# Kernel tuning notes

Hardware: AMD Instinct MI355X
Metric: run time of the kernel (lower is better)

Reference implementation:

```python
import jax, jax.numpy as jnp
import numpy as np


def setup_inputs() -> dict:
    key = jax.random.key(0)
    ks = jax.random.split(key, 7)
    B, N, F, H = 128, 64, 128, 128
    s1 = 1.0 / np.sqrt(2 * N)  # torch Linear default-ish scaling
    s2 = 1.0 / np.sqrt(H)
    return {
        "agent_features": jax.random.normal(ks[0], (B, N, F), dtype=jnp.float32),
        "W1": jax.random.normal(ks[1], (2 * N, H), dtype=jnp.float32) * s1,
        "b1": jax.random.normal(ks[2], (H,), dtype=jnp.float32) * s1,
        "W2": jax.random.normal(ks[3], (H, H), dtype=jnp.float32) * s2,
        "b2": jax.random.normal(ks[4], (H,), dtype=jnp.float32) * s2,
        "w3": jax.random.normal(ks[5], (H,), dtype=jnp.float32) * s2,
        "b3": jax.random.normal(ks[6], (1,), dtype=jnp.float32) * s2,
        "mixing_weights": jnp.ones((N,), dtype=jnp.float32) / N,
    }


def reference(agent_features, W1, b1, W2, b2, w3, b3, mixing_weights):
    N = mixing_weights.shape[0]
    f = agent_features[:, :, :N]  # [B, N, N] (first num_agents features)
    # Split first Linear's weight into the i-half and j-half of the concat:
    # concat([f_i, f_j]) @ W1 == f_i @ W1[:N] + f_j @ W1[N:]
    Ai = jnp.einsum('bnf,fh->bnh', f, W1[:N])   # contribution of agent i
    Aj = jnp.einsum('bnf,fh->bnh', f, W1[N:])   # contribution of agent j
    h1 = jax.nn.relu(Ai[:, :, None, :] + Aj[:, None, :, :] + b1)  # [B,N,N,H]
    h2 = jax.nn.relu(jnp.einsum('bijh,hk->bijk', h1, W2) + b2)    # [B,N,N,H]
    correlations = jax.nn.sigmoid(jnp.einsum('bijh,h->bij', h2, w3) + b3[0])
    weights = jax.nn.softmax(mixing_weights, axis=0)
    return correlations, weights
```

## Files before the change

### kernel.cpp

```cpp
#include <hip/hip_runtime.h>
#include <hip/hip_bf16.h>


typedef __bf16 bf16x8 __attribute__((ext_vector_type(8)));
typedef float f32x4 __attribute__((ext_vector_type(4)));

#define B_SZ 128
#define N_SZ 64
#define H_SZ 128

__global__ __launch_bounds__(256) void setup_kernel(
    const float* __restrict__ af, const float* __restrict__ W1,
    const float* __restrict__ b1, const float* __restrict__ W2,
    const float* __restrict__ mw, float* __restrict__ AiP,
    float* __restrict__ Aj, unsigned short* __restrict__ W2T,
    float* __restrict__ outw)
{
  const int blk = blockIdx.x;
  const int tid = threadIdx.x;

  if (blk < 2048) {
    __shared__ float fl[4 * 64];
    const int bn0 = blk << 2;
    fl[tid] = af[((bn0 + (tid >> 6)) << 7) + (tid & 63)];
    __syncthreads();
    const int h    = tid & 127;
    const int half = tid >> 7;
    const float* Wp = W1 + ((half << 6) << 7) + h;
    float acc0 = 0.f, acc1 = 0.f, acc2 = 0.f, acc3 = 0.f;
#pragma unroll
    for (int fq = 0; fq < 16; ++fq) {
      const float w0 = Wp[(fq * 4 + 0) << 7];
      const float w1v = Wp[(fq * 4 + 1) << 7];
      const float w2v = Wp[(fq * 4 + 2) << 7];
      const float w3v = Wp[(fq * 4 + 3) << 7];
      const float4 f0 = *(const float4*)&fl[0 * 64 + (fq << 2)];
      const float4 f1 = *(const float4*)&fl[1 * 64 + (fq << 2)];
      const float4 f2 = *(const float4*)&fl[2 * 64 + (fq << 2)];
      const float4 f3 = *(const float4*)&fl[3 * 64 + (fq << 2)];
      acc0 = fmaf(f0.x, w0, fmaf(f0.y, w1v, fmaf(f0.z, w2v, fmaf(f0.w, w3v, acc0))));
      acc1 = fmaf(f1.x, w0, fmaf(f1.y, w1v, fmaf(f1.z, w2v, fmaf(f1.w, w3v, acc1))));
      acc2 = fmaf(f2.x, w0, fmaf(f2.y, w1v, fmaf(f2.z, w2v, fmaf(f2.w, w3v, acc2))));
      acc3 = fmaf(f3.x, w0, fmaf(f3.y, w1v, fmaf(f3.z, w2v, fmaf(f3.w, w3v, acc3))));
    }
    if (half == 0) {
      const float bb = b1[h];
      AiP[((bn0 + 0) << 7) + h] = acc0 + bb;
      AiP[((bn0 + 1) << 7) + h] = acc1 + bb;
      AiP[((bn0 + 2) << 7) + h] = acc2 + bb;
      AiP[((bn0 + 3) << 7) + h] = acc3 + bb;
    } else {
      Aj[((bn0 + 0) << 7) + h] = acc0;
      Aj[((bn0 + 1) << 7) + h] = acc1;
      Aj[((bn0 + 2) << 7) + h] = acc2;
      Aj[((bn0 + 3) << 7) + h] = acc3;
    }
  } else if (blk < 2112) {
    int idx = ((blk - 2048) << 8) + tid;
    int k = idx >> 7, n = idx & 127;
    unsigned u = __float_as_uint(W2[idx]);
    u += 0x7fffu + ((u >> 16) & 1u);
    W2T[(n << 7) + k] = (unsigned short)(u >> 16);
  } else {
    if (tid < 64) {
      float v = mw[tid];
      float m = v;
      for (int off = 32; off > 0; off >>= 1) m = fmaxf(m, __shfl_xor(m, off));
      float e = expf(v - m);
      float s = e;
      for (int off = 32; off > 0; off >>= 1) s += __shfl_xor(s, off);
      outw[tid] = e / s;
    }
  }
}

__global__ __launch_bounds__(512, 2) void corr_kernel(
    const float* __restrict__ AiP, const float* __restrict__ Aj,
    const unsigned short* __restrict__ W2T,
    const float* __restrict__ b2, const float* __restrict__ w3,
    const float* __restrict__ b3, float* __restrict__ out)
{
  __shared__ __align__(16) unsigned short W2s[128 * 128];
  __shared__ __align__(16) float AjF[64 * 132];
  __shared__ __align__(16) float AiF[32 * 132];
  __shared__ float b2s[128], w3s[128];
  __shared__ float part[2][2][128];

  const int tid  = threadIdx.x;
  const int lane = tid & 63;
  const int wave = tid >> 6;
  const int c = lane & 15, g = lane >> 4;
  const int wm = wave & 1;
  const int wn = wave >> 1;

  const int blk = blockIdx.x;
  const int b   = blk >> 1;
  const int ih  = blk & 1;
  const int ip0 = ih << 4;

  {
    const uint4* src = (const uint4*)W2T;
#pragma unroll
    for (int it = 0; it < 4; ++it) {
      const int idx = (it << 9) + tid;
      const int n = idx >> 4, e = idx & 15;
      const uint4 v = src[idx];
      *(uint4*)&W2s[(n << 7) + ((e ^ (n & 15)) << 3)] = v;
    }
  }
  {
    const float4* src = (const float4*)(Aj + (b << 13));
#pragma unroll
    for (int p = 0; p < 4; ++p) {
      const int idx = (p << 9) + tid;
      const int r = idx >> 5, u = idx & 31;
      *(float4*)&AjF[r * 132 + (u << 2)] = src[idx];
    }
    const float4* srcA = (const float4*)(AiP + (((b << 6) + (ih << 5)) << 7));
#pragma unroll
    for (int p = 0; p < 2; ++p) {
      const int idx = (p << 9) + tid;
      const int r = idx >> 5, u = idx & 31;
      *(float4*)&AiF[r * 132 + (u << 2)] = srcA[idx];
    }
    if (tid < 128) b2s[tid] = b2[tid];
    else if (tid < 256) w3s[tid - 128] = w3[tid - 128];
  }

  const float bias3 = b3[0];
  const int i_sel = wn >> 1;

  __syncthreads();

  bf16x8 w2r[4][4];
#pragma unroll
  for (int mt = 0; mt < 4; ++mt)
#pragma unroll
    for (int kt = 0; kt < 4; ++kt) {
      const int es = ((kt << 2) + g) ^ c;
      w2r[mt][kt] = *(const bf16x8*)&W2s[(((wm << 6) + (mt << 4) + c) << 7) + (es << 3)];
    }
  f32x4 ajr[4][2][2];
#pragma unroll
  for (int kt = 0; kt < 4; ++kt)
#pragma unroll
    for (int tn = 0; tn < 2; ++tn) {
      const int j = ((wn << 5) + (tn << 4) + c) & 63;
      const float* ajb = &AjF[j * 132 + (g << 3) + (kt << 5)];
      ajr[kt][tn][0] = *(const f32x4*)(ajb);
      ajr[kt][tn][1] = *(const f32x4*)(ajb + 4);
    }

  for (int t = 0; t < 16; ++t) {
    const float* aib = &AiF[((t << 1) + i_sel) * 132 + (g << 3)];

    f32x4 acc[4][2];
#pragma unroll
    for (int mt = 0; mt < 4; ++mt) {
      const f32x4 bv = *(const f32x4*)&b2s[(wm << 6) + (mt << 4) + (g << 2)];
      acc[mt][0] = bv;
      acc[mt][1] = bv;
    }

#pragma unroll
    for (int kt = 0; kt < 4; ++kt) {
      const f32x4 a0 = *(const f32x4*)(aib + (kt << 5));
      const f32x4 a1 = *(const f32x4*)(aib + (kt << 5) + 4);
      bf16x8 hv[2];
#pragma unroll
      for (int tn = 0; tn < 2; ++tn) {
        const f32x4 h0 = a0 + ajr[kt][tn][0];
        const f32x4 h1v = a1 + ajr[kt][tn][1];
#pragma unroll
        for (int e = 0; e < 4; ++e) {
          hv[tn][e]     = (__bf16)fmaxf(h0[e], 0.f);
          hv[tn][e + 4] = (__bf16)fmaxf(h1v[e], 0.f);
        }
      }
#pragma unroll
      for (int mt = 0; mt < 4; ++mt)
#pragma unroll
        for (int tn = 0; tn < 2; ++tn)
          acc[mt][tn] = __builtin_amdgcn_mfma_f32_16x16x32_bf16(
              w2r[mt][kt], hv[tn], acc[mt][tn], 0, 0, 0);
    }

    float s0 = 0.f, s1 = 0.f;
#pragma unroll
    for (int mt = 0; mt < 4; ++mt) {
      const f32x4 wv3 = *(const f32x4*)&w3s[(wm << 6) + (mt << 4) + (g << 2)];
#pragma unroll
      for (int p = 0; p < 4; ++p) {
        s0 = fmaf(fmaxf(acc[mt][0][p], 0.f), wv3[p], s0);
        s1 = fmaf(fmaxf(acc[mt][1][p], 0.f), wv3[p], s1);
      }
    }
    s0 += __shfl_xor(s0, 16);
    s0 += __shfl_xor(s0, 32);
    s1 += __shfl_xor(s1, 16);
    s1 += __shfl_xor(s1, 32);

    const int pb = t & 1;
    if (g == 0) {
      part[pb][wm][(wn << 5) + c]      = s0;
      part[pb][wm][(wn << 5) + 16 + c] = s1;
    }

    __syncthreads();

    if (tid < 128) {
      const float v = part[pb][0][tid] + part[pb][1][tid] + bias3;
      out[(b << 12) + ((ip0 + t) << 7) + tid] = 1.f / (1.f + __expf(-v));
    }
  }
}

extern "C" void kernel_launch(void* const* d_in, const int* in_sizes, int n_in,
                              void* d_out, int out_size, void* d_ws,
                              size_t ws_size, hipStream_t stream)
{
  const float* af = (const float*)d_in[0];
  const float* W1 = (const float*)d_in[1];
  const float* b1 = (const float*)d_in[2];
  const float* W2 = (const float*)d_in[3];
  const float* b2 = (const float*)d_in[4];
  const float* w3 = (const float*)d_in[5];
  const float* b3 = (const float*)d_in[6];
  const float* mw = (const float*)d_in[7];
  float* out = (float*)d_out;

  float* AiP = (float*)d_ws;
  float* Aj  = AiP + B_SZ * N_SZ * H_SZ;
  unsigned short* W2T = (unsigned short*)(Aj + B_SZ * N_SZ * H_SZ);

  setup_kernel<<<2113, 256, 0, stream>>>(af, W1, b1, W2, mw, AiP, Aj, W2T,
                                         out + B_SZ * N_SZ * N_SZ);
  corr_kernel<<<256, 512, 0, stream>>>(AiP, Aj, W2T, b2, w3, b3, out);
}
```

Measured before the change: 102.9 us.

## Fuse first-layer projection and W2 conversion into the correlation kernel

Merges the setup kernel into the main kernel. Each block now computes its own Aj (all 64 rows) and Ai (its 32 rows) projections from agent features in shared memory, and loads W2 straight from global memory, converting it to bf16 into registers. This removes a kernel launch and the workspace round trip for AiP, Aj and W2T. In exchange, each batch's Aj projection is computed twice (once per i-half block), and every block does strided fp32 reads of W2 and W1 through a 64-entry register array, which may raise register pressure.

After: 105.7 us. 1.03x slower.

```diff
diff --git a/kernel.cpp b/kernel.cpp
--- a/kernel.cpp
+++ b/kernel.cpp
@@ -5,82 +5,14 @@
 typedef __bf16 bf16x8 __attribute__((ext_vector_type(8)));
 typedef float f32x4 __attribute__((ext_vector_type(4)));
 
-#define B_SZ 128
-#define N_SZ 64
-#define H_SZ 128
-
-__global__ __launch_bounds__(256) void setup_kernel(
+__global__ __launch_bounds__(512, 2) void fused_kernel(
     const float* __restrict__ af, const float* __restrict__ W1,
     const float* __restrict__ b1, const float* __restrict__ W2,
-    const float* __restrict__ mw, float* __restrict__ AiP,
-    float* __restrict__ Aj, unsigned short* __restrict__ W2T,
-    float* __restrict__ outw)
+    const float* __restrict__ b2, const float* __restrict__ w3,
+    const float* __restrict__ b3, const float* __restrict__ mw,
+    float* __restrict__ out)
 {
-  const int blk = blockIdx.x;
-  const int tid = threadIdx.x;
-
-  if (blk < 2048) {
-    __shared__ float fl[4 * 64];
-    const int bn0 = blk << 2;
-    fl[tid] = af[((bn0 + (tid >> 6)) << 7) + (tid & 63)];
-    __syncthreads();
-    const int h    = tid & 127;
-    const int half = tid >> 7;
-    const float* Wp = W1 + ((half << 6) << 7) + h;
-    float acc0 = 0.f, acc1 = 0.f, acc2 = 0.f, acc3 = 0.f;
-#pragma unroll
-    for (int fq = 0; fq < 16; ++fq) {
-      const float w0 = Wp[(fq * 4 + 0) << 7];
-      const float w1v = Wp[(fq * 4 + 1) << 7];
-      const float w2v = Wp[(fq * 4 + 2) << 7];
-      const float w3v = Wp[(fq * 4 + 3) << 7];
-      const float4 f0 = *(const float4*)&fl[0 * 64 + (fq << 2)];
-      const float4 f1 = *(const float4*)&fl[1 * 64 + (fq << 2)];
-      const float4 f2 = *(const float4*)&fl[2 * 64 + (fq << 2)];
-      const float4 f3 = *(const float4*)&fl[3 * 64 + (fq << 2)];
-      acc0 = fmaf(f0.x, w0, fmaf(f0.y, w1v, fmaf(f0.z, w2v, fmaf(f0.w, w3v, acc0))));
-      acc1 = fmaf(f1.x, w0, fmaf(f1.y, w1v, fmaf(f1.z, w2v, fmaf(f1.w, w3v, acc1))));
-      acc2 = fmaf(f2.x, w0, fmaf(f2.y, w1v, fmaf(f2.z, w2v, fmaf(f2.w, w3v, acc2))));
-      acc3 = fmaf(f3.x, w0, fmaf(f3.y, w1v, fmaf(f3.z, w2v, fmaf(f3.w, w3v, acc3))));
-    }
-    if (half == 0) {
-      const float bb = b1[h];
-      AiP[((bn0 + 0) << 7) + h] = acc0 + bb;
-      AiP[((bn0 + 1) << 7) + h] = acc1 + bb;
-      AiP[((bn0 + 2) << 7) + h] = acc2 + bb;
-      AiP[((bn0 + 3) << 7) + h] = acc3 + bb;
-    } else {
-      Aj[((bn0 + 0) << 7) + h] = acc0;
-      Aj[((bn0 + 1) << 7) + h] = acc1;
-      Aj[((bn0 + 2) << 7) + h] = acc2;
-      Aj[((bn0 + 3) << 7) + h] = acc3;
-    }
-  } else if (blk < 2112) {
-    int idx = ((blk - 2048) << 8) + tid;
-    int k = idx >> 7, n = idx & 127;
-    unsigned u = __float_as_uint(W2[idx]);
-    u += 0x7fffu + ((u >> 16) & 1u);
-    W2T[(n << 7) + k] = (unsigned short)(u >> 16);
-  } else {
-    if (tid < 64) {
-      float v = mw[tid];
-      float m = v;
-      for (int off = 32; off > 0; off >>= 1) m = fmaxf(m, __shfl_xor(m, off));
-      float e = expf(v - m);
-      float s = e;
-      for (int off = 32; off > 0; off >>= 1) s += __shfl_xor(s, off);
-      outw[tid] = e / s;
-    }
-  }
-}
-
-__global__ __launch_bounds__(512, 2) void corr_kernel(
-    const float* __restrict__ AiP, const float* __restrict__ Aj,
-    const unsigned short* __restrict__ W2T,
-    const float* __restrict__ b2, const float* __restrict__ w3,
-    const float* __restrict__ b3, float* __restrict__ out)
-{
-  __shared__ __align__(16) unsigned short W2s[128 * 128];
+  __shared__ __align__(16) float fl[64 * 64];
   __shared__ __align__(16) float AjF[64 * 132];
   __shared__ __align__(16) float AiF[32 * 132];
   __shared__ float b2s[128], w3s[128];
@@ -98,48 +30,113 @@
   const int ih  = blk & 1;
   const int ip0 = ih << 4;
 
+  if (blk == 0 && tid < 64) {
+    float v = mw[tid];
+    float m = v;
+    for (int off = 32; off > 0; off >>= 1) m = fmaxf(m, __shfl_xor(m, off));
+    float e = expf(v - m);
+    float s = e;
+    for (int off = 32; off > 0; off >>= 1) s += __shfl_xor(s, off);
+    out[128 * 64 * 64 + tid] = e / s;
+  }
+
   {
-    const uint4* src = (const uint4*)W2T;
-#pragma unroll
-    for (int it = 0; it < 4; ++it) {
-      const int idx = (it << 9) + tid;
-      const int n = idx >> 4, e = idx & 15;
-      const uint4 v = src[idx];
-      *(uint4*)&W2s[(n << 7) + ((e ^ (n & 15)) << 3)] = v;
-    }
-  }
-  {
-    const float4* src = (const float4*)(Aj + (b << 13));
-#pragma unroll
-    for (int p = 0; p < 4; ++p) {
-      const int idx = (p << 9) + tid;
-      const int r = idx >> 5, u = idx & 31;
-      *(float4*)&AjF[r * 132 + (u << 2)] = src[idx];
-    }
-    const float4* srcA = (const float4*)(AiP + (((b << 6) + (ih << 5)) << 7));
+    const float4* srcQ = (const float4*)(af + (b << 13));
 #pragma unroll
     for (int p = 0; p < 2; ++p) {
       const int idx = (p << 9) + tid;
-      const int r = idx >> 5, u = idx & 31;
-      *(float4*)&AiF[r * 132 + (u << 2)] = srcA[idx];
+      const int n = idx >> 4, e = idx & 15;
+      *(float4*)&fl[(n << 6) + (e << 2)] = srcQ[(n << 5) + e];
     }
     if (tid < 128) b2s[tid] = b2[tid];
     else if (tid < 256) w3s[tid - 128] = w3[tid - 128];
   }
 
+  bf16x8 w2r[4][4];
+  {
+    union U { unsigned short s; __bf16 h; };
+#pragma unroll
+    for (int mt = 0; mt < 4; ++mt)
+#pragma unroll
+      for (int kt = 0; kt < 4; ++kt) {
+        const float* wp = W2 + (((kt << 5) + (g << 3)) << 7) +
+                          (wm << 6) + (mt << 4) + c;
+#pragma unroll
+        for (int e = 0; e < 8; ++e) {
+          unsigned u = __float_as_uint(wp[e << 7]);
+          u += 0x7fffu + ((u >> 16) & 1u);
+          U cv; cv.s = (unsigned short)(u >> 16);
+          w2r[mt][kt][e] = cv.h;
+        }
+      }
+  }
+
+  const int h = tid & 127;
+  const int q = tid >> 7;
+  const float b1h = b1[h];
   const float bias3 = b3[0];
-  const int i_sel = wn >> 1;
 
   __syncthreads();
 
-  bf16x8 w2r[4][4];
-#pragma unroll
-  for (int mt = 0; mt < 4; ++mt)
-#pragma unroll
-    for (int kt = 0; kt < 4; ++kt) {
-      const int es = ((kt << 2) + g) ^ c;
-      w2r[mt][kt] = *(const bf16x8*)&W2s[(((wm << 6) + (mt << 4) + c) << 7) + (es << 3)];
-    }
+  {
+    float w1c[64];
+#pragma unroll
+    for (int f = 0; f < 64; ++f) w1c[f] = W1[((64 + f) << 7) + h];
+#pragma unroll
+    for (int qd = 0; qd < 4; ++qd) {
+      const int r0 = (q << 4) + (qd << 2);
+      float a0 = 0.f, a1 = 0.f, a2 = 0.f, a3 = 0.f;
+#pragma unroll
+      for (int fq = 0; fq < 16; ++fq) {
+        const float w0  = w1c[fq * 4 + 0];
+        const float w1v = w1c[fq * 4 + 1];
+        const float w2v = w1c[fq * 4 + 2];
+        const float w3v = w1c[fq * 4 + 3];
+        const float4 f0 = *(const float4*)&fl[((r0 + 0) << 6) + (fq << 2)];
+        const float4 f1 = *(const float4*)&fl[((r0 + 1) << 6) + (fq << 2)];
+        const float4 f2 = *(const float4*)&fl[((r0 + 2) << 6) + (fq << 2)];
+        const float4 f3 = *(const float4*)&fl[((r0 + 3) << 6) + (fq << 2)];
+        a0 = fmaf(f0.x, w0, fmaf(f0.y, w1v, fmaf(f0.z, w2v, fmaf(f0.w, w3v, a0))));
+        a1 = fmaf(f1.x, w0, fmaf(f1.y, w1v, fmaf(f1.z, w2v, fmaf(f1.w, w3v, a1))));
+        a2 = fmaf(f2.x, w0, fmaf(f2.y, w1v, fmaf(f2.z, w2v, fmaf(f2.w, w3v, a2))));
+        a3 = fmaf(f3.x, w0, fmaf(f3.y, w1v, fmaf(f3.z, w2v, fmaf(f3.w, w3v, a3))));
+      }
+      AjF[(r0 + 0) * 132 + h] = a0;
+      AjF[(r0 + 1) * 132 + h] = a1;
+      AjF[(r0 + 2) * 132 + h] = a2;
+      AjF[(r0 + 3) * 132 + h] = a3;
+    }
+#pragma unroll
+    for (int f = 0; f < 64; ++f) w1c[f] = W1[(f << 7) + h];
+#pragma unroll
+    for (int qd = 0; qd < 2; ++qd) {
+      const int r0 = (q << 3) + (qd << 2);
+      const int fr = (ih << 5) + r0;
+      float a0 = 0.f, a1 = 0.f, a2 = 0.f, a3 = 0.f;
+#pragma unroll
+      for (int fq = 0; fq < 16; ++fq) {
+        const float w0  = w1c[fq * 4 + 0];
+        const float w1v = w1c[fq * 4 + 1];
+        const float w2v = w1c[fq * 4 + 2];
+        const float w3v = w1c[fq * 4 + 3];
+        const float4 f0 = *(const float4*)&fl[((fr + 0) << 6) + (fq << 2)];
+        const float4 f1 = *(const float4*)&fl[((fr + 1) << 6) + (fq << 2)];
+        const float4 f2 = *(const float4*)&fl[((fr + 2) << 6) + (fq << 2)];
+        const float4 f3 = *(const float4*)&fl[((fr + 3) << 6) + (fq << 2)];
+        a0 = fmaf(f0.x, w0, fmaf(f0.y, w1v, fmaf(f0.z, w2v, fmaf(f0.w, w3v, a0))));
+        a1 = fmaf(f1.x, w0, fmaf(f1.y, w1v, fmaf(f1.z, w2v, fmaf(f1.w, w3v, a1))));
+        a2 = fmaf(f2.x, w0, fmaf(f2.y, w1v, fmaf(f2.z, w2v, fmaf(f2.w, w3v, a2))));
+        a3 = fmaf(f3.x, w0, fmaf(f3.y, w1v, fmaf(f3.z, w2v, fmaf(f3.w, w3v, a3))));
+      }
+      AiF[(r0 + 0) * 132 + h] = a0 + b1h;
+      AiF[(r0 + 1) * 132 + h] = a1 + b1h;
+      AiF[(r0 + 2) * 132 + h] = a2 + b1h;
+      AiF[(r0 + 3) * 132 + h] = a3 + b1h;
+    }
+  }
+
+  __syncthreads();
+
   f32x4 ajr[4][2][2];
 #pragma unroll
   for (int kt = 0; kt < 4; ++kt)
@@ -151,6 +148,8 @@
       ajr[kt][tn][1] = *(const f32x4*)(ajb + 4);
     }
 
+  const int i_sel = wn >> 1;
+
   for (int t = 0; t < 16; ++t) {
     const float* aib = &AiF[((t << 1) + i_sel) * 132 + (g << 3)];
 
@@ -169,7 +168,7 @@
       bf16x8 hv[2];
 #pragma unroll
       for (int tn = 0; tn < 2; ++tn) {
-        const f32x4 h0 = a0 + ajr[kt][tn][0];
+        const f32x4 h0  = a0 + ajr[kt][tn][0];
         const f32x4 h1v = a1 + ajr[kt][tn][1];
 #pragma unroll
         for (int e = 0; e < 4; ++e) {
@@ -229,11 +228,6 @@
   const float* mw = (const float*)d_in[7];
   float* out = (float*)d_out;
 
-  float* AiP = (float*)d_ws;
-  float* Aj  = AiP + B_SZ * N_SZ * H_SZ;
-  unsigned short* W2T = (unsigned short*)(Aj + B_SZ * N_SZ * H_SZ);
-
-  setup_kernel<<<2113, 256, 0, stream>>>(af, W1, b1, W2, mw, AiP, Aj, W2T,
-                                         out + B_SZ * N_SZ * N_SZ);
-  corr_kernel<<<256, 512, 0, stream>>>(AiP, Aj, W2T, b2, w3, b3, out);
+  (void)d_ws; (void)ws_size;
+  fused_kernel<<<256, 512, 0, stream>>>(af, W1, b1, W2, b2, w3, b3, mw, out);
 }
```
